# Kernel tuning notes

Hardware: AMD Instinct MI355X
Metric: run time of the kernel (lower is better)

The kernel has to match this reference:

```python
import jax, jax.numpy as jnp
import numpy as np

N, E, F, H, C, G = 100000, 1600000, 128, 128, 10, 1024


def setup_inputs() -> dict:
    key = jax.random.key(0)
    ks = jax.random.split(key, 8)
    s = 0.05
    return {
        "x": jax.random.normal(ks[0], (N, F), dtype=jnp.float32),
        "edge_index": jax.random.randint(ks[1], (2, E), 0, N, dtype=jnp.int64),
        "batch": jnp.sort(jax.random.randint(ks[2], (N,), 0, G, dtype=jnp.int64)),
        "num_graphs": G,
        "W1": jax.random.normal(ks[3], (F, H), dtype=jnp.float32) * s,
        "b1": jnp.zeros((H,), jnp.float32),
        "W2": jax.random.normal(ks[4], (H, H), dtype=jnp.float32) * s,
        "b2": jnp.zeros((H,), jnp.float32),
        "W3": jax.random.normal(ks[5], (H, H), dtype=jnp.float32) * s,
        "b3": jnp.zeros((H,), jnp.float32),
        "Wo": jax.random.normal(ks[6], (H, C), dtype=jnp.float32) * s,
        "bo": jnp.zeros((C,), jnp.float32),
    }


def reference(x, edge_index, batch, num_graphs, W1, b1, W2, b2, W3, b3, Wo, bo):
    n = x.shape[0]
    loops = jnp.arange(n, dtype=edge_index.dtype)
    # GCNConv adds self-loops, then sym-normalizes: D^-1/2 (A+I) D^-1/2
    src = jnp.concatenate([edge_index[0], loops])
    dst = jnp.concatenate([edge_index[1], loops])
    deg = jax.ops.segment_sum(jnp.ones_like(src, dtype=x.dtype), dst, num_segments=n)
    dinv = jnp.where(deg > 0, jax.lax.rsqrt(jnp.maximum(deg, 1e-12)), 0.0)
    norm = (dinv[src] * dinv[dst])[:, None]  # [E+N, 1]

    h = x
    for W, b in ((W1, b1), (W2, b2), (W3, b3)):
        hw = h @ W  # small GEMM, [N, H]
        agg = jax.ops.segment_sum(hw[src] * norm, dst, num_segments=n)  # gather+scatter
        h = jax.nn.relu(agg + b)  # norm layer is Identity (net_norm='none')

    # global_mean_pool over graphs
    sums = jax.ops.segment_sum(h, batch, num_segments=num_graphs)
    cnt = jax.ops.segment_sum(jnp.ones((n,), h.dtype), batch, num_segments=num_graphs)
    pooled = sums / jnp.maximum(cnt, 1.0)[:, None]  # [G, H]

    return jax.nn.log_softmax(pooled @ Wo + bo, axis=-1)  # [G, C]
```

## Files before the change

kernel.cpp:

```cpp
#include <hip/hip_runtime.h>
#include <hip/hip_bf16.h>
#include <stdint.h>

#define FDIM 128
#define CDIM 10

typedef unsigned short u16;
typedef unsigned char u8;
typedef __attribute__((ext_vector_type(8))) short short8;
typedef __attribute__((ext_vector_type(4))) float f32x4;
typedef __attribute__((ext_vector_type(2))) float f32x2;

__device__ inline u16 f2bf(float f) {
    unsigned int u = __float_as_uint(f);
    u += 0x7fff + ((u >> 16) & 1);
    return (u16)(u >> 16);
}
__device__ inline unsigned int pack2(float a, float b) {
    return (unsigned int)f2bf(a) | ((unsigned int)f2bf(b) << 16);
}
__device__ inline void acc_fp8x4(f32x2& a0, f32x2& a1, unsigned u) {
    a0 += __builtin_amdgcn_cvt_pk_f32_fp8(u, false);
    a1 += __builtin_amdgcn_cvt_pk_f32_fp8(u, true);
}
__device__ inline unsigned pk_fp8x4(float a, float b, float c, float d) {
    unsigned o = 0;
    o = __builtin_amdgcn_cvt_pk_fp8_f32(a, b, o, false);
    o = __builtin_amdgcn_cvt_pk_fp8_f32(c, d, o, true);
    return o;
}


__global__ void sentinel_kernel(float* __restrict__ out, int n, float val) {
    int i = blockIdx.x * blockDim.x + threadIdx.x;
    if (i < n) out[i] = val;
}

__global__ void wconv_kernel(const float* __restrict__ W1, const float* __restrict__ W2,
                             const float* __restrict__ W3, u16* __restrict__ wbt,
                             unsigned* __restrict__ hs8A_rowN, unsigned* __restrict__ hs8B_rowN,
                             int* __restrict__ bcnt, int NB) {
    int tid = threadIdx.x;
    if (blockIdx.x == 192) {
        if (tid < FDIM / 4) { hs8A_rowN[tid] = 0; hs8B_rowN[tid] = 0; }
        return;
    }
    if (blockIdx.x == 193) {
        for (int i = tid; i < NB; i += 256) bcnt[i] = 0;
        return;
    }
    int which = blockIdx.x >> 6;
    int i = (blockIdx.x & 63) * 256 + tid;
    const float* W = which == 0 ? W1 : (which == 1 ? W2 : W3);
    int k = i >> 7, n = i & 127;
    wbt[(size_t)which * 16384 + n * 128 + k] = f2bf(W[k * 128 + n]);
}

__global__ void xconv_kernel(const float* __restrict__ x, const float* __restrict__ dinv,
                             u8* __restrict__ hs8A, int N) {
    int i = (blockIdx.x * blockDim.x + threadIdx.x) * 4;
    if (i < N * FDIM) {
        int v = i >> 7;
        float dv = dinv[v];
        float4 f = *(const float4*)&x[i];
        ((unsigned*)hs8A)[i >> 2] = pk_fp8x4(dv * f.x, dv * f.y, dv * f.z, dv * f.w);
    }
}


#define ECHUNK 2048

__global__ __launch_bounds__(256) void count_kernel(const int* __restrict__ dst, int E,
                                                    int* __restrict__ bcnt, int NB) {
    __shared__ int lc[1024];
    int tid = threadIdx.x;
    for (int i = tid; i < NB; i += 256) lc[i] = 0;
    __syncthreads();
    int base = blockIdx.x * ECHUNK;
    int lim = min(base + ECHUNK, E);
    for (int i = base + tid; i < lim; i += 256)
        atomicAdd(&lc[dst[i] >> 7], 1);
    __syncthreads();
    for (int i = tid; i < NB; i += 256)
        if (lc[i]) atomicAdd(&bcnt[i], lc[i]);
}

__global__ __launch_bounds__(1024) void scan_kernel(const int* __restrict__ bcnt, int NB, int E,
                                                    int* __restrict__ boff, int* __restrict__ bcursor) {
    __shared__ int s[1024];
    int tid = threadIdx.x;
    s[tid] = (tid < NB) ? bcnt[tid] : 0;
    __syncthreads();
    for (int off = 1; off < 1024; off <<= 1) {
        int v = (tid >= off) ? s[tid - off] : 0;
        __syncthreads();
        s[tid] += v;
        __syncthreads();
    }
    int excl = tid ? s[tid - 1] : 0;
    if (tid < NB) { boff[tid] = excl; bcursor[tid] = excl; }
    if (tid == 0) boff[NB] = E;
}

__global__ __launch_bounds__(256) void part_kernel(const int* __restrict__ src,
                                                   const int* __restrict__ dst, int E,
                                                   int* __restrict__ bcursor,
                                                   unsigned* __restrict__ ebuf, int NB) {
    __shared__ int lc[1024];
    __shared__ int lbase[1024];
    int tid = threadIdx.x;
    for (int i = tid; i < NB; i += 256) lc[i] = 0;
    __syncthreads();
    int base = blockIdx.x * ECHUNK;
    int lim = min(base + ECHUNK, E);
    for (int i = base + tid; i < lim; i += 256)
        atomicAdd(&lc[dst[i] >> 7], 1);
    __syncthreads();
    for (int i = tid; i < NB; i += 256) {
        int c = lc[i];
        lbase[i] = c ? atomicAdd(&bcursor[i], c) : 0;
        lc[i] = 0;
    }
    __syncthreads();
    for (int i = base + tid; i < lim; i += 256) {
        int s_ = src[i];
        int d_ = dst[i];
        int b = d_ >> 7;
        int r = atomicAdd(&lc[b], 1);
        ebuf[lbase[b] + r] = ((unsigned)(d_ & 127) << 25) | (unsigned)s_;
    }
}

__global__ __launch_bounds__(256) void build_kernel(const unsigned* __restrict__ ebuf,
                                                    const int* __restrict__ boff,
                                                    int* __restrict__ rowp, float* __restrict__ dinv,
                                                    int* __restrict__ colx, int N, int E) {
    __shared__ int hist[128];
    __shared__ int pfx[128];
    __shared__ int cur[128];
    int b = blockIdx.x;
    int tid = threadIdx.x;
    int ebase = boff[b], eend = boff[b + 1];
    if (tid < 128) hist[tid] = 0;
    __syncthreads();
    for (int i = ebase + tid; i < eend; i += 256)
        atomicAdd(&hist[ebuf[i] >> 25], 1);
    __syncthreads();
    if (tid < 128) {
        int deg = hist[tid];
        pfx[tid] = deg;
    }
    __syncthreads();
    for (int off = 1; off < 128; off <<= 1) {
        int t = 0;
        if (tid < 128 && tid >= off) t = pfx[tid - off];
        __syncthreads();
        if (tid < 128) pfx[tid] += t;
        __syncthreads();
    }
    if (tid < 128) {
        int deg = hist[tid];
        int excl = pfx[tid] - deg;
        int node = b * 128 + tid;
        if (node < N) {
            rowp[node] = ebase + excl;
            dinv[node] = rsqrtf(1.0f + (float)deg);
            if (node == N - 1) rowp[N] = E;
        }
        cur[tid] = ebase + excl;
    }
    __syncthreads();
    for (int i = ebase + tid; i < eend; i += 256) {
        unsigned e = ebuf[i];
        int r = atomicAdd(&cur[e >> 25], 1);
        colx[r] = (int)(e & 0x1FFFFFFu);
    }
}


template <bool FP8OUT>
__global__ __launch_bounds__(256) void layer_kernel(const u8* __restrict__ hs8_in,
                                                    const int* __restrict__ rowp,
                                                    const int* __restrict__ colx,
                                                    const float* __restrict__ dinv,
                                                    const u16* __restrict__ WbT,
                                                    const float* __restrict__ bias,
                                                    u8* __restrict__ out8,
                                                    u16* __restrict__ outbf, int N) {
    __shared__ u16 As[64][136];
    __shared__ u8 As8[64][144];
    int tid = threadIdx.x;
    int w = tid >> 6;
    int l = tid & 63;
    int row0 = blockIdx.x * 64;
    int grp = tid >> 3;
    int c = tid & 7;
    const uint4* h4 = (const uint4*)hs8_in;

#pragma unroll
    for (int p = 0; p < 2; ++p) {
        int r = p * 32 + grp;
        int v = row0 + r;
        uint4 o0 = make_uint4(0, 0, 0, 0), o1 = make_uint4(0, 0, 0, 0);
        if (v < N) {
            f32x2 acc[8];
            uint4 s = h4[(size_t)v * 8 + c];
#pragma unroll
            for (int j = 0; j < 8; ++j) acc[j] = (f32x2){0.f, 0.f};
            acc_fp8x4(acc[0], acc[1], s.x); acc_fp8x4(acc[2], acc[3], s.y);
            acc_fp8x4(acc[4], acc[5], s.z); acc_fp8x4(acc[6], acc[7], s.w);
            int e = rowp[v], end = rowp[v + 1];
            for (; e + 2 <= end; e += 2) {
                int u0 = colx[e];
                int u1 = colx[e + 1];
                uint4 r0 = h4[(size_t)u0 * 8 + c];
                uint4 r1 = h4[(size_t)u1 * 8 + c];
                acc_fp8x4(acc[0], acc[1], r0.x); acc_fp8x4(acc[2], acc[3], r0.y);
                acc_fp8x4(acc[4], acc[5], r0.z); acc_fp8x4(acc[6], acc[7], r0.w);
                acc_fp8x4(acc[0], acc[1], r1.x); acc_fp8x4(acc[2], acc[3], r1.y);
                acc_fp8x4(acc[4], acc[5], r1.z); acc_fp8x4(acc[6], acc[7], r1.w);
            }
            if (e < end) {
                int u = colx[e];
                uint4 rr = h4[(size_t)u * 8 + c];
                acc_fp8x4(acc[0], acc[1], rr.x); acc_fp8x4(acc[2], acc[3], rr.y);
                acc_fp8x4(acc[4], acc[5], rr.z); acc_fp8x4(acc[6], acc[7], rr.w);
            }
            float dv = dinv[v];
            o0.x = pack2(dv * acc[0].x, dv * acc[0].y);
            o0.y = pack2(dv * acc[1].x, dv * acc[1].y);
            o0.z = pack2(dv * acc[2].x, dv * acc[2].y);
            o0.w = pack2(dv * acc[3].x, dv * acc[3].y);
            o1.x = pack2(dv * acc[4].x, dv * acc[4].y);
            o1.y = pack2(dv * acc[5].x, dv * acc[5].y);
            o1.z = pack2(dv * acc[6].x, dv * acc[6].y);
            o1.w = pack2(dv * acc[7].x, dv * acc[7].y);
        }
        *(uint4*)&As[r][c * 16] = o0;
        *(uint4*)&As[r][c * 16 + 8] = o1;
    }
    __syncthreads();

    int arow = w * 16 + (l & 15);
    int kblk = (l >> 4) * 8;
    f32x4 facc[8];
#pragma unroll
    for (int f = 0; f < 8; ++f) facc[f] = (f32x4){0.f, 0.f, 0.f, 0.f};

#pragma unroll
    for (int kk = 0; kk < 4; ++kk) {
        int k0 = kk * 32 + kblk;
        short8 a = *(const short8*)&As[arow][k0];
#pragma unroll
        for (int f = 0; f < 8; ++f) {
            int col = f * 16 + (l & 15);
            short8 bfr = *(const short8*)&WbT[(size_t)col * FDIM + k0];
            facc[f] = __builtin_amdgcn_mfma_f32_16x16x32_bf16(a, bfr, facc[f], 0, 0, 0);
        }
    }

    int rbase = w * 16 + (l >> 4) * 4;
    int cidx = l & 15;

    if constexpr (FP8OUT) {
        float dvr[4];
#pragma unroll
        for (int r = 0; r < 4; ++r) {
            int row = row0 + rbase + r;
            dvr[r] = (row < N) ? dinv[row] : 1.f;
        }
#pragma unroll
        for (int f = 0; f < 8; ++f) {
            int col = f * 16 + cidx;
            float bv = bias[col];
#pragma unroll
            for (int r = 0; r < 4; ++r) {
                float val = dvr[r] * fmaxf(facc[f][r] + bv, 0.f);
                unsigned pk = __builtin_amdgcn_cvt_pk_fp8_f32(val, 0.f, 0, false);
                As8[rbase + r][col] = (u8)(pk & 0xff);
            }
        }
#pragma unroll
        for (int i = 0; i < 2; ++i) {
            int flat = i * 64 + l;
            int r = w * 16 + (flat >> 3);
            int ch = flat & 7;
            if (row0 + r < N)
                ((uint4*)(out8 + (size_t)(row0 + r) * FDIM))[ch] = *(const uint4*)&As8[r][ch * 16];
        }
    } else {
#pragma unroll
        for (int f = 0; f < 8; ++f) {
            int col = f * 16 + cidx;
            float bv = bias[col];
#pragma unroll
            for (int r = 0; r < 4; ++r)
                As[rbase + r][col] = f2bf(fmaxf(facc[f][r] + bv, 0.f));
        }
#pragma unroll
        for (int i = 0; i < 4; ++i) {
            int r = w * 16 + (l >> 4) * 4 + i;
            int col = (l & 15) * 8;
            if (row0 + r < N) *(uint4*)&outbf[(size_t)(row0 + r) * FDIM + col] = *(const uint4*)&As[r][col];
        }
    }
}


__global__ __launch_bounds__(512) void pool_head_kernel(const u16* __restrict__ h,
                                                        const int* __restrict__ batch, int N,
                                                        const float* __restrict__ Wo,
                                                        const float* __restrict__ bo,
                                                        float* __restrict__ out, int G) {
    int g = blockIdx.x;
    int tid = threadIdx.x;
    __shared__ int bounds[2];
    __shared__ float2 red[512];
    __shared__ float sp[128];
    __shared__ float lg[CDIM];
    __shared__ float sm[2];

    if (tid < 2) {
        int target = g + tid;
        int lo = 0, hi = N;
        while (lo < hi) {
            int mid = (lo + hi) >> 1;
            if (batch[mid] < target) lo = mid + 1; else hi = mid;
        }
        bounds[tid] = lo;
    }
    __syncthreads();
    int lo = bounds[0], hi = bounds[1];
    int cnt = hi - lo;

    int j = tid & 63;
    int rg = tid >> 6;
    const unsigned* h2 = (const unsigned*)h;
    float ax = 0.f, ay = 0.f;
    for (int r = lo + rg; r < hi; r += 8) {
        unsigned u = h2[(size_t)r * 64 + j];
        ax += __uint_as_float(u << 16);
        ay += __uint_as_float(u & 0xffff0000u);
    }
    red[tid] = make_float2(ax, ay);
    __syncthreads();
    if (tid < 64) {
        float sx = 0.f, sy = 0.f;
#pragma unroll
        for (int k = 0; k < 8; ++k) {
            float2 t = red[tid + 64 * k];
            sx += t.x; sy += t.y;
        }
        float inv = 1.f / (float)max(cnt, 1);
        sp[2 * tid] = sx * inv;
        sp[2 * tid + 1] = sy * inv;
    }
    __syncthreads();

    if (tid < CDIM) {
        float l = bo[tid];
        for (int k = 0; k < 128; ++k) l += sp[k] * Wo[(size_t)k * CDIM + tid];
        lg[tid] = l;
    }
    __syncthreads();
    if (tid == 0) {
        float m = -1e30f;
        for (int c = 0; c < CDIM; ++c) m = fmaxf(m, lg[c]);
        float ssum = 0.f;
        for (int c = 0; c < CDIM; ++c) ssum += expf(lg[c] - m);
        sm[0] = m;
        sm[1] = logf(ssum);
    }
    __syncthreads();
    if (tid < CDIM) out[(size_t)g * CDIM + tid] = lg[tid] - sm[0] - sm[1];
}


extern "C" void kernel_launch(void* const* d_in, const int* in_sizes, int n_in,
                              void* d_out, int out_size, void* d_ws, size_t ws_size,
                              hipStream_t stream) {
    const float* x = (const float*)d_in[0];
    const int* edge = (const int*)d_in[1];
    const int* batch = (const int*)d_in[2];
    const float* W1 = (const float*)d_in[4];
    const float* b1 = (const float*)d_in[5];
    const float* W2 = (const float*)d_in[6];
    const float* b2 = (const float*)d_in[7];
    const float* W3 = (const float*)d_in[8];
    const float* b3 = (const float*)d_in[9];
    const float* Wo = (const float*)d_in[10];
    const float* bo = (const float*)d_in[11];

    int N = in_sizes[2];
    int E = in_sizes[1] / 2;
    int G = out_size / CDIM;
    const int* src = edge;
    const int* dst = edge + E;
    int NB = (N + 127) >> 7;

    size_t off = 0;
    auto carve = [&](size_t bytes) -> size_t {
        size_t r = off;
        off += (bytes + 255) & ~(size_t)255;
        return r;
    };
    size_t o_h3   = carve((size_t)N * FDIM * 2);
    size_t o_hs8A = carve((size_t)(N + 1) * FDIM);
    size_t o_hs8B = carve((size_t)(N + 1) * FDIM);
    size_t o_colx = carve((size_t)E * 4);
    size_t o_rowp = carve((size_t)(N + 1) * 4);
    size_t o_dinv = carve((size_t)N * 4);
    size_t o_bcnt = carve((size_t)NB * 4);
    size_t o_boff = carve((size_t)(NB + 1) * 4);
    size_t o_bcur = carve((size_t)NB * 4);
    size_t o_wbt  = carve((size_t)3 * 16384 * 2);

    bool ok = off <= ws_size && NB <= 1024 && N <= (1 << 25) &&
              (size_t)E * 4 <= (size_t)N * FDIM * 2;
    if (!ok) {
        sentinel_kernel<<<(out_size + 255) / 256, 256, 0, stream>>>((float*)d_out, out_size, 1234.5f);
        return;
    }

    char* base = (char*)d_ws;
    u16* h3bf  = (u16*)(base + o_h3);
    u8* hs8A   = (u8*)(base + o_hs8A);
    u8* hs8B   = (u8*)(base + o_hs8B);
    unsigned* ebuf = (unsigned*)(base + o_h3);
    int* colx  = (int*)(base + o_colx);
    int* rowp  = (int*)(base + o_rowp);
    float* dinv = (float*)(base + o_dinv);
    int* bcnt  = (int*)(base + o_bcnt);
    int* boff  = (int*)(base + o_boff);
    int* bcur  = (int*)(base + o_bcur);
    u16* wbt   = (u16*)(base + o_wbt);

    int nchunk = (E + ECHUNK - 1) / ECHUNK;

    wconv_kernel<<<194, 256, 0, stream>>>(W1, W2, W3, wbt,
                                          (unsigned*)(hs8A + (size_t)N * FDIM),
                                          (unsigned*)(hs8B + (size_t)N * FDIM), bcnt, NB);
    count_kernel<<<nchunk, 256, 0, stream>>>(dst, E, bcnt, NB);
    scan_kernel<<<1, 1024, 0, stream>>>(bcnt, NB, E, boff, bcur);
    part_kernel<<<nchunk, 256, 0, stream>>>(src, dst, E, bcur, ebuf, NB);
    build_kernel<<<NB, 256, 0, stream>>>(ebuf, boff, rowp, dinv, colx, N, E);
    xconv_kernel<<<(N * FDIM / 4 + 255) / 256, 256, 0, stream>>>(x, dinv, hs8A, N);

    int layerBlocks = (N + 63) / 64;

    layer_kernel<true><<<layerBlocks, 256, 0, stream>>>(hs8A, rowp, colx, dinv, wbt, b1, hs8B, nullptr, N);
    layer_kernel<true><<<layerBlocks, 256, 0, stream>>>(hs8B, rowp, colx, dinv, wbt + 16384, b2, hs8A, nullptr, N);
    layer_kernel<false><<<layerBlocks, 256, 0, stream>>>(hs8A, rowp, colx, dinv, wbt + 32768, b3, nullptr, h3bf, N);

    pool_head_kernel<<<G, 512, 0, stream>>>(h3bf, batch, N, Wo, bo, (float*)d_out, G);
}
```

Before: 315.2 us.

## Split fused layer into degree-sorted aggregation and separate MFMA GEMM kernels

Each fused aggregate+GEMM layer kernel becomes two kernels: a gather aggregation that writes an fp8 intermediate, and an MFMA GEMM that reads it. The aggregation visits nodes in an order bucketed by degree, using a permutation built from a degree histogram in the build kernel plus new scan and scatter kernels. The aim is to balance gather work across the lanes of a wavefront and to decouple the GEMM from irregular gather latency. In exchange it adds a write and re-read of an N×128 fp8 intermediate per layer, an extra fp8 rounding of the aggregate, and several extra launches.

```diff
diff --git a/kernel.cpp b/kernel.cpp
--- a/kernel.cpp
+++ b/kernel.cpp
@@ -38,11 +38,12 @@
 
 __global__ void wconv_kernel(const float* __restrict__ W1, const float* __restrict__ W2,
                              const float* __restrict__ W3, u16* __restrict__ wbt,
-                             unsigned* __restrict__ hs8A_rowN, unsigned* __restrict__ hs8B_rowN,
+                             unsigned* __restrict__ hs8A_rowN, int* __restrict__ dbin,
                              int* __restrict__ bcnt, int NB) {
     int tid = threadIdx.x;
     if (blockIdx.x == 192) {
-        if (tid < FDIM / 4) { hs8A_rowN[tid] = 0; hs8B_rowN[tid] = 0; }
+        if (tid < FDIM / 4) hs8A_rowN[tid] = 0;
+        if (tid < 256) dbin[tid] = 0;
         return;
     }
     if (blockIdx.x == 193) {
@@ -134,22 +135,22 @@
 __global__ __launch_bounds__(256) void build_kernel(const unsigned* __restrict__ ebuf,
                                                     const int* __restrict__ boff,
                                                     int* __restrict__ rowp, float* __restrict__ dinv,
-                                                    int* __restrict__ colx, int N, int E) {
+                                                    int* __restrict__ colx, int* __restrict__ dbin,
+                                                    int N, int E) {
     __shared__ int hist[128];
     __shared__ int pfx[128];
     __shared__ int cur[128];
+    __shared__ int ldbin[256];
     int b = blockIdx.x;
     int tid = threadIdx.x;
     int ebase = boff[b], eend = boff[b + 1];
     if (tid < 128) hist[tid] = 0;
+    ldbin[tid] = 0;
     __syncthreads();
     for (int i = ebase + tid; i < eend; i += 256)
         atomicAdd(&hist[ebuf[i] >> 25], 1);
     __syncthreads();
-    if (tid < 128) {
-        int deg = hist[tid];
-        pfx[tid] = deg;
-    }
+    if (tid < 128) pfx[tid] = hist[tid];
     __syncthreads();
     for (int off = 1; off < 128; off <<= 1) {
         int t = 0;
@@ -166,6 +167,7 @@
             rowp[node] = ebase + excl;
             dinv[node] = rsqrtf(1.0f + (float)deg);
             if (node == N - 1) rowp[N] = E;
+            atomicAdd(&ldbin[min(deg, 255)], 1);
         }
         cur[tid] = ebase + excl;
     }
@@ -175,69 +177,125 @@
         int r = atomicAdd(&cur[e >> 25], 1);
         colx[r] = (int)(e & 0x1FFFFFFu);
     }
+    if (ldbin[tid]) atomicAdd(&dbin[tid], ldbin[tid]);
+}
+
+__global__ __launch_bounds__(256) void dscan_kernel(const int* __restrict__ dbin,
+                                                    int* __restrict__ dcur) {
+    __shared__ int s[256];
+    int tid = threadIdx.x;
+    s[tid] = dbin[tid];
+    __syncthreads();
+    for (int off = 1; off < 256; off <<= 1) {
+        int v = (tid >= off) ? s[tid - off] : 0;
+        __syncthreads();
+        s[tid] += v;
+        __syncthreads();
+    }
+    dcur[tid] = tid ? s[tid - 1] : 0;
+}
+
+__global__ __launch_bounds__(256) void dscatter_kernel(const int* __restrict__ rowp,
+                                                       int* __restrict__ dcur,
+                                                       int* __restrict__ perm, int N) {
+    int i = blockIdx.x * blockDim.x + threadIdx.x;
+    if (i < N) {
+        int deg = rowp[i + 1] - rowp[i];
+        int slot = atomicAdd(&dcur[min(deg, 255)], 1);
+        perm[slot] = i;
+    }
+}
+
+
+__global__ __launch_bounds__(256) void agg_kernel(const u8* __restrict__ hs8,
+                                                  const float* __restrict__ dinv,
+                                                  const int* __restrict__ rowp,
+                                                  const int* __restrict__ colx,
+                                                  const int* __restrict__ perm,
+                                                  u8* __restrict__ out8, int N) {
+    int tid = threadIdx.x;
+    int lane = tid & 63;
+    int g = lane >> 3;
+    int c = lane & 7;
+    int idx = blockIdx.x * 32 + (tid >> 6) * 8 + g;
+    bool valid = idx < N;
+    int v = valid ? perm[idx] : N;
+
+    const uint4* h4 = (const uint4*)hs8;
+    f32x2 acc[8];
+    uint4 s = h4[(size_t)v * 8 + c];
+#pragma unroll
+    for (int j = 0; j < 8; ++j) acc[j] = (f32x2){0.f, 0.f};
+    acc_fp8x4(acc[0], acc[1], s.x); acc_fp8x4(acc[2], acc[3], s.y);
+    acc_fp8x4(acc[4], acc[5], s.z); acc_fp8x4(acc[6], acc[7], s.w);
+
+    int e = valid ? rowp[v] : 0;
+    int end = valid ? rowp[v + 1] : 0;
+    for (; e + 2 <= end; e += 2) {
+        int u0 = colx[e];
+        int u1 = colx[e + 1];
+        uint4 r0 = h4[(size_t)u0 * 8 + c];
+        uint4 r1 = h4[(size_t)u1 * 8 + c];
+        acc_fp8x4(acc[0], acc[1], r0.x); acc_fp8x4(acc[2], acc[3], r0.y);
+        acc_fp8x4(acc[4], acc[5], r0.z); acc_fp8x4(acc[6], acc[7], r0.w);
+        acc_fp8x4(acc[0], acc[1], r1.x); acc_fp8x4(acc[2], acc[3], r1.y);
+        acc_fp8x4(acc[4], acc[5], r1.z); acc_fp8x4(acc[6], acc[7], r1.w);
+    }
+    if (e < end) {
+        int u = colx[e];
+        uint4 r = h4[(size_t)u * 8 + c];
+        acc_fp8x4(acc[0], acc[1], r.x); acc_fp8x4(acc[2], acc[3], r.y);
+        acc_fp8x4(acc[4], acc[5], r.z); acc_fp8x4(acc[6], acc[7], r.w);
+    }
+
+    if (valid) {
+        float dv = dinv[v];
+        uint4 o;
+        o.x = pk_fp8x4(dv * acc[0].x, dv * acc[0].y, dv * acc[1].x, dv * acc[1].y);
+        o.y = pk_fp8x4(dv * acc[2].x, dv * acc[2].y, dv * acc[3].x, dv * acc[3].y);
+        o.z = pk_fp8x4(dv * acc[4].x, dv * acc[4].y, dv * acc[5].x, dv * acc[5].y);
+        o.w = pk_fp8x4(dv * acc[6].x, dv * acc[6].y, dv * acc[7].x, dv * acc[7].y);
+        ((uint4*)out8)[(size_t)v * 8 + c] = o;
+    }
 }
 
 
 template <bool FP8OUT>
-__global__ __launch_bounds__(256) void layer_kernel(const u8* __restrict__ hs8_in,
-                                                    const int* __restrict__ rowp,
-                                                    const int* __restrict__ colx,
-                                                    const float* __restrict__ dinv,
-                                                    const u16* __restrict__ WbT,
-                                                    const float* __restrict__ bias,
-                                                    u8* __restrict__ out8,
-                                                    u16* __restrict__ outbf, int N) {
+__global__ __launch_bounds__(256) void gemm_mfma_kernel(const u8* __restrict__ in8,
+                                                        const u16* __restrict__ WbT,
+                                                        const float* __restrict__ bias,
+                                                        const float* __restrict__ dinv,
+                                                        u8* __restrict__ out8,
+                                                        u16* __restrict__ outbf, int N) {
     __shared__ u16 As[64][136];
     __shared__ u8 As8[64][144];
     int tid = threadIdx.x;
     int w = tid >> 6;
     int l = tid & 63;
     int row0 = blockIdx.x * 64;
-    int grp = tid >> 3;
-    int c = tid & 7;
-    const uint4* h4 = (const uint4*)hs8_in;
-
-#pragma unroll
-    for (int p = 0; p < 2; ++p) {
-        int r = p * 32 + grp;
-        int v = row0 + r;
-        uint4 o0 = make_uint4(0, 0, 0, 0), o1 = make_uint4(0, 0, 0, 0);
-        if (v < N) {
-            f32x2 acc[8];
-            uint4 s = h4[(size_t)v * 8 + c];
-#pragma unroll
-            for (int j = 0; j < 8; ++j) acc[j] = (f32x2){0.f, 0.f};
-            acc_fp8x4(acc[0], acc[1], s.x); acc_fp8x4(acc[2], acc[3], s.y);
-            acc_fp8x4(acc[4], acc[5], s.z); acc_fp8x4(acc[6], acc[7], s.w);
-            int e = rowp[v], end = rowp[v + 1];
-            for (; e + 2 <= end; e += 2) {
-                int u0 = colx[e];
-                int u1 = colx[e + 1];
-                uint4 r0 = h4[(size_t)u0 * 8 + c];
-                uint4 r1 = h4[(size_t)u1 * 8 + c];
-                acc_fp8x4(acc[0], acc[1], r0.x); acc_fp8x4(acc[2], acc[3], r0.y);
-                acc_fp8x4(acc[4], acc[5], r0.z); acc_fp8x4(acc[6], acc[7], r0.w);
-                acc_fp8x4(acc[0], acc[1], r1.x); acc_fp8x4(acc[2], acc[3], r1.y);
-                acc_fp8x4(acc[4], acc[5], r1.z); acc_fp8x4(acc[6], acc[7], r1.w);
-            }
-            if (e < end) {
-                int u = colx[e];
-                uint4 rr = h4[(size_t)u * 8 + c];
-                acc_fp8x4(acc[0], acc[1], rr.x); acc_fp8x4(acc[2], acc[3], rr.y);
-                acc_fp8x4(acc[4], acc[5], rr.z); acc_fp8x4(acc[6], acc[7], rr.w);
-            }
-            float dv = dinv[v];
-            o0.x = pack2(dv * acc[0].x, dv * acc[0].y);
-            o0.y = pack2(dv * acc[1].x, dv * acc[1].y);
-            o0.z = pack2(dv * acc[2].x, dv * acc[2].y);
-            o0.w = pack2(dv * acc[3].x, dv * acc[3].y);
-            o1.x = pack2(dv * acc[4].x, dv * acc[4].y);
-            o1.y = pack2(dv * acc[5].x, dv * acc[5].y);
-            o1.z = pack2(dv * acc[6].x, dv * acc[6].y);
-            o1.w = pack2(dv * acc[7].x, dv * acc[7].y);
-        }
-        *(uint4*)&As[r][c * 16] = o0;
-        *(uint4*)&As[r][c * 16 + 8] = o1;
+
+#pragma unroll
+    for (int i = 0; i < 2; ++i) {
+        int ch = tid + 256 * i;
+        int r = ch >> 3;
+        int cc = ch & 7;
+        uint4 val = make_uint4(0, 0, 0, 0);
+        if (row0 + r < N) val = ((const uint4*)(in8 + (size_t)(row0 + r) * FDIM))[cc];
+        f32x2 f0 = __builtin_amdgcn_cvt_pk_f32_fp8(val.x, false);
+        f32x2 f1 = __builtin_amdgcn_cvt_pk_f32_fp8(val.x, true);
+        f32x2 f2 = __builtin_amdgcn_cvt_pk_f32_fp8(val.y, false);
+        f32x2 f3 = __builtin_amdgcn_cvt_pk_f32_fp8(val.y, true);
+        f32x2 f4 = __builtin_amdgcn_cvt_pk_f32_fp8(val.z, false);
+        f32x2 f5 = __builtin_amdgcn_cvt_pk_f32_fp8(val.z, true);
+        f32x2 f6 = __builtin_amdgcn_cvt_pk_f32_fp8(val.w, false);
+        f32x2 f7 = __builtin_amdgcn_cvt_pk_f32_fp8(val.w, true);
+        uint4 o0, o1;
+        o0.x = pack2(f0.x, f0.y); o0.y = pack2(f1.x, f1.y);
+        o0.z = pack2(f2.x, f2.y); o0.w = pack2(f3.x, f3.y);
+        o1.x = pack2(f4.x, f4.y); o1.y = pack2(f5.x, f5.y);
+        o1.z = pack2(f6.x, f6.y); o1.w = pack2(f7.x, f7.y);
+        *(uint4*)&As[r][cc * 16] = o0;
+        *(uint4*)&As[r][cc * 16 + 8] = o1;
     }
     __syncthreads();
 
@@ -406,13 +464,16 @@
     };
     size_t o_h3   = carve((size_t)N * FDIM * 2);
     size_t o_hs8A = carve((size_t)(N + 1) * FDIM);
-    size_t o_hs8B = carve((size_t)(N + 1) * FDIM);
+    size_t o_agg8 = carve((size_t)N * FDIM);
     size_t o_colx = carve((size_t)E * 4);
     size_t o_rowp = carve((size_t)(N + 1) * 4);
     size_t o_dinv = carve((size_t)N * 4);
+    size_t o_perm = carve((size_t)N * 4);
     size_t o_bcnt = carve((size_t)NB * 4);
     size_t o_boff = carve((size_t)(NB + 1) * 4);
     size_t o_bcur = carve((size_t)NB * 4);
+    size_t o_dbin = carve(256 * 4);
+    size_t o_dcur = carve(256 * 4);
     size_t o_wbt  = carve((size_t)3 * 16384 * 2);
 
     bool ok = off <= ws_size && NB <= 1024 && N <= (1 << 25) &&
@@ -425,32 +486,40 @@
     char* base = (char*)d_ws;
     u16* h3bf  = (u16*)(base + o_h3);
     u8* hs8A   = (u8*)(base + o_hs8A);
-    u8* hs8B   = (u8*)(base + o_hs8B);
+    u8* agg8   = (u8*)(base + o_agg8);
     unsigned* ebuf = (unsigned*)(base + o_h3);
     int* colx  = (int*)(base + o_colx);
     int* rowp  = (int*)(base + o_rowp);
     float* dinv = (float*)(base + o_dinv);
+    int* perm  = (int*)(base + o_perm);
     int* bcnt  = (int*)(base + o_bcnt);
     int* boff  = (int*)(base + o_boff);
     int* bcur  = (int*)(base + o_bcur);
+    int* dbin  = (int*)(base + o_dbin);
+    int* dcur  = (int*)(base + o_dcur);
     u16* wbt   = (u16*)(base + o_wbt);
 
     int nchunk = (E + ECHUNK - 1) / ECHUNK;
 
     wconv_kernel<<<194, 256, 0, stream>>>(W1, W2, W3, wbt,
-                                          (unsigned*)(hs8A + (size_t)N * FDIM),
-                                          (unsigned*)(hs8B + (size_t)N * FDIM), bcnt, NB);
+                                          (unsigned*)(hs8A + (size_t)N * FDIM), dbin, bcnt, NB);
     count_kernel<<<nchunk, 256, 0, stream>>>(dst, E, bcnt, NB);
     scan_kernel<<<1, 1024, 0, stream>>>(bcnt, NB, E, boff, bcur);
     part_kernel<<<nchunk, 256, 0, stream>>>(src, dst, E, bcur, ebuf, NB);
-    build_kernel<<<NB, 256, 0, stream>>>(ebuf, boff, rowp, dinv, colx, N, E);
+    build_kernel<<<NB, 256, 0, stream>>>(ebuf, boff, rowp, dinv, colx, dbin, N, E);
+    dscan_kernel<<<1, 256, 0, stream>>>(dbin, dcur);
+    dscatter_kernel<<<(N + 255) / 256, 256, 0, stream>>>(rowp, dcur, perm, N);
     xconv_kernel<<<(N * FDIM / 4 + 255) / 256, 256, 0, stream>>>(x, dinv, hs8A, N);
 
-    int layerBlocks = (N + 63) / 64;
-
-    layer_kernel<true><<<layerBlocks, 256, 0, stream>>>(hs8A, rowp, colx, dinv, wbt, b1, hs8B, nullptr, N);
-    layer_kernel<true><<<layerBlocks, 256, 0, stream>>>(hs8B, rowp, colx, dinv, wbt + 16384, b2, hs8A, nullptr, N);
-    layer_kernel<false><<<layerBlocks, 256, 0, stream>>>(hs8A, rowp, colx, dinv, wbt + 32768, b3, nullptr, h3bf, N);
+    int aggBlocks = (N + 31) / 32;
+    int gemmBlocks = (N + 63) / 64;
+
+    agg_kernel<<<aggBlocks, 256, 0, stream>>>(hs8A, dinv, rowp, colx, perm, agg8, N);
+    gemm_mfma_kernel<true><<<gemmBlocks, 256, 0, stream>>>(agg8, wbt, b1, dinv, hs8A, nullptr, N);
+    agg_kernel<<<aggBlocks, 256, 0, stream>>>(hs8A, dinv, rowp, colx, perm, agg8, N);
+    gemm_mfma_kernel<true><<<gemmBlocks, 256, 0, stream>>>(agg8, wbt + 16384, b2, dinv, hs8A, nullptr, N);
+    agg_kernel<<<aggBlocks, 256, 0, stream>>>(hs8A, dinv, rowp, colx, perm, agg8, N);
+    gemm_mfma_kernel<false><<<gemmBlocks, 256, 0, stream>>>(agg8, wbt + 32768, b3, dinv, nullptr, h3bf, N);
 
     pool_head_kernel<<<G, 512, 0, stream>>>(h3bf, batch, N, Wo, bo, (float*)d_out, G);
 }
```

Measured after the change: 585.1 us. 85.6% more time.
